# Kernel tuning notes

Hardware: AMD Instinct MI355X
Metric: run time of the kernel (lower is better)

The kernel has to match this reference:

```python
import jax, jax.numpy as jnp
import numpy as np

N = 50000        # nodes
R = 51           # enriched relations (25 fwd + 25 inverse + self-loop)
F_IN = 32        # feat_size
E = 32           # embed_size
C = 16           # num_classes
B = 30           # num_bases
NNZ = 2_000_000  # nonzeros in vertical adjacency


def _xavier(key, shape):
    # mimics nn.init.xavier_uniform_ with gain for relu (sqrt(2))
    fan_in, fan_out = shape[-2], shape[-1]
    a = np.sqrt(2.0) * np.sqrt(6.0 / (fan_in + fan_out))
    return jax.random.uniform(key, shape, jnp.float32, -a, a)


def setup_inputs() -> dict:
    key = jax.random.key(0)
    ks = jax.random.split(key, 8)
    # COO of vertical adjacency, shape (R*N, N)
    rows = jax.random.randint(ks[0], (NNZ,), 0, R * N)
    cols = jax.random.randint(ks[1], (NNZ,), 0, N)
    # row-normalized values: vals = 1 / row_degree  (sum_sparse with rows=True)
    deg = jax.ops.segment_sum(jnp.ones((NNZ,), jnp.float32), rows, num_segments=R * N)
    vals = (1.0 / jnp.maximum(deg, 1.0))[rows]
    features = jax.random.normal(ks[2], (N, F_IN), jnp.float32)
    comps1 = _xavier(ks[3], (R, B))
    bases1 = _xavier(ks[4], (B, F_IN, E))
    comps2 = _xavier(ks[5], (R, B))
    bases2 = _xavier(ks[6], (B, E, C))
    bias1 = jnp.zeros((E,), jnp.float32)
    bias2 = jnp.zeros((C,), jnp.float32)
    return {
        "features": features, "vals": vals,
        "comps1": comps1, "bases1": bases1, "bias1": bias1,
        "comps2": comps2, "bases2": bases2, "bias2": bias2,
        "rows": rows, "cols": cols,
    }


def _spmm(rows, cols, vals, x):
    # (R*N, N) sparse @ (N, f) dense -> (R*N, f)
    return jax.ops.segment_sum(vals[:, None] * x[cols], rows, num_segments=R * N)


def reference(features, vals, comps1, bases1, bias1, comps2, bases2, bias2, rows, cols):
    # layer 1: SpMM then basis-decomposed per-relation mixing
    h = _spmm(rows, cols, vals, features).reshape(R, N, F_IN)   # (r, n, f)
    w1 = jnp.einsum('rb,bfe->rfe', comps1, bases1)              # (r, f, e)
    h = jnp.einsum('rnf,rfe->ne', h, w1)                        # (n, e)
    h = jax.nn.relu(h + bias1)
    # layer 2
    h = _spmm(rows, cols, vals, h).reshape(R, N, E)             # (r, n, e)
    w2 = jnp.einsum('rb,bho->rho', comps2, bases2)              # (r, e, c)
    h = jnp.einsum('rho,rnh->no', w2, h)                        # (n, c)
    return h + bias2
```

## Files before the change

### kernel.cpp

```cpp
#include <hip/hip_runtime.h>

#define NNODES 50000
#define RREL 51
#define FIN 32
#define EDIM 32
#define CDIM 16
#define BB 30
#define NNZ_ 2000000
#define EPB 4096
#define NBUK 391
#define PCAP_MAX 2800128

typedef unsigned int uint32;
typedef unsigned short ushort;
typedef uint32 u32x2 __attribute__((ext_vector_type(2)));
typedef uint32 u32x4 __attribute__((ext_vector_type(4)));
typedef short bf16x8 __attribute__((ext_vector_type(8)));
typedef float f32x4 __attribute__((ext_vector_type(4)));
typedef float f32x16 __attribute__((ext_vector_type(16)));

static __device__ __forceinline__ uint32 pack_bf16x2(float a, float b) {
    uint32 ua = __builtin_bit_cast(uint32, a);
    uint32 ub = __builtin_bit_cast(uint32, b);
    ua += 0x7fffu + ((ua >> 16) & 1u);
    ub += 0x7fffu + ((ub >> 16) & 1u);
    return (ua >> 16) | (ub & 0xffff0000u);
}
static __device__ __forceinline__ ushort bf16_1(float x) {
    uint32 u = __builtin_bit_cast(uint32, x);
    u += 0x7fffu + ((u >> 16) & 1u);
    return (ushort)(u >> 16);
}

__global__ void k_weights2(const float* __restrict__ bases1, const float* __restrict__ bases2,
                           ushort* __restrict__ Wb1, ushort* __restrict__ Wb2) {
    int i = blockIdx.x * 256 + threadIdx.x;
    if (i < 960 * 32) {
        int e = i & 31, k = i >> 5;
        int b = k >> 5, f = k & 31;
        float v = bases1[b * 1024 + f * 32 + e];
        Wb1[((k >> 3) * 32 + e) * 8 + (k & 7)] = bf16_1(v);
    }
    if (i < 960 * 16) {
        int e = i & 15, k = i >> 4;
        int b = k >> 5, h = k & 31;
        float v = bases2[b * 512 + h * 16 + e];
        Wb2[((k >> 3) * 16 + e) * 8 + (k & 7)] = bf16_1(v);
    }
}

__global__ void k_tobf16(const float2* __restrict__ src, uint32* __restrict__ dst, int n2) {
    int i = blockIdx.x * 256 + threadIdx.x;
    if (i < n2) {
        float2 f = src[i];
        dst[i] = pack_bf16x2(f.x, f.y);
    }
}

__global__ __launch_bounds__(1024) void k_bukhist(const int* __restrict__ rows,
                                                  int* __restrict__ buk_cnt) {
    __shared__ int lc[NBUK];
    int t = threadIdx.x;
    if (t < NBUK) lc[t] = 0;
    __syncthreads();
    size_t k = (size_t)blockIdx.x * EPB + (size_t)t * 4;
    int rr[4];
    if (k + 4 <= NNZ_) {
        int4 rw = *(const int4*)(rows + k);
        rr[0] = rw.x; rr[1] = rw.y; rr[2] = rw.z; rr[3] = rw.w;
    } else {
#pragma unroll
        for (int j = 0; j < 4; j++) rr[j] = (k + j < NNZ_) ? rows[k + j] : -1;
    }
#pragma unroll
    for (int j = 0; j < 4; j++)
        if (rr[j] >= 0) {
            int rel = rr[j] / NNODES;
            int dst = rr[j] - rel * NNODES;
            atomicAdd(&lc[dst >> 7], 1);
        }
    __syncthreads();
    if (t < NBUK) atomicAdd(&buk_cnt[t], lc[t]);
}

__global__ void k_scan1(const int* __restrict__ buk_cnt, int* __restrict__ buk_base,
                        int* __restrict__ buk_cur) {
    if (threadIdx.x == 0) {
        int a = 0;
        for (int b = 0; b < NBUK; b++) { buk_base[b] = a; buk_cur[b] = a; a += buk_cnt[b]; }
        buk_base[NBUK] = a;
    }
}

__global__ __launch_bounds__(1024) void k_bucket2(const int* __restrict__ rows,
                                                  const int* __restrict__ cols,
                                                  const float* __restrict__ vals,
                                                  int* __restrict__ buk_cur,
                                                  u32x2* __restrict__ tok8,
                                                  float* __restrict__ sval_b) {
    __shared__ int bukc[NBUK], lb[NBUK], gb[NBUK];
    __shared__ int ssum[1024];
    __shared__ u32x2 st8[EPB];
    __shared__ float sv[EPB];
    int t = threadIdx.x;
    size_t base = (size_t)blockIdx.x * EPB;
    int total = (int)(((size_t)NNZ_ - base < (size_t)EPB) ? ((size_t)NNZ_ - base) : (size_t)EPB);
    if (t < NBUK) bukc[t] = 0;
    __syncthreads();
    size_t k = base + (size_t)t * 4;
    int bv[4]; uint32 tx[4], ty[4]; float vv[4];
    if (k + 4 <= NNZ_) {
        int4 rw = *(const int4*)(rows + k);
        int4 cw = *(const int4*)(cols + k);
        float4 vw = *(const float4*)(vals + k);
        int rr[4] = {rw.x, rw.y, rw.z, rw.w};
        int cc[4] = {cw.x, cw.y, cw.z, cw.w};
        vv[0] = vw.x; vv[1] = vw.y; vv[2] = vw.z; vv[3] = vw.w;
#pragma unroll
        for (int j = 0; j < 4; j++) {
            int rel = rr[j] / NNODES;
            int dst = rr[j] - rel * NNODES;
            bv[j] = dst >> 7;
            tx[j] = (uint32)dst | ((uint32)rel << 16);
            ty[j] = (uint32)cc[j] | ((uint32)rel << 16);
        }
    } else {
#pragma unroll
        for (int j = 0; j < 4; j++) {
            if (k + j < NNZ_) {
                int r = rows[k + j];
                int rel = r / NNODES;
                int dst = r - rel * NNODES;
                bv[j] = dst >> 7;
                tx[j] = (uint32)dst | ((uint32)rel << 16);
                ty[j] = (uint32)cols[k + j] | ((uint32)rel << 16);
                vv[j] = vals[k + j];
            } else bv[j] = -1;
        }
    }
#pragma unroll
    for (int j = 0; j < 4; j++)
        if (bv[j] >= 0) atomicAdd(&bukc[bv[j]], 1);
    __syncthreads();
    int v = (t < NBUK) ? bukc[t] : 0;
    ssum[t] = v;
    __syncthreads();
    for (int off = 1; off < 1024; off <<= 1) {
        int u = (t >= off) ? ssum[t - off] : 0;
        __syncthreads();
        ssum[t] += u;
        __syncthreads();
    }
    if (t < NBUK) { lb[t] = ssum[t] - v; gb[t] = atomicAdd(&buk_cur[t], v); }
    __syncthreads();
    if (t < NBUK) bukc[t] = 0;
    __syncthreads();
#pragma unroll
    for (int j = 0; j < 4; j++) {
        if (bv[j] >= 0) {
            int slot = lb[bv[j]] + atomicAdd(&bukc[bv[j]], 1);
            u32x2 w; w.x = tx[j]; w.y = ty[j];
            st8[slot] = w;
            sv[slot] = vv[j];
        }
    }
    __syncthreads();
    for (int s = t; s < total; s += 1024) {
        u32x2 w = st8[s];
        int bk = (int)((w.x & 0xFFFFu) >> 7);
        int pos = gb[bk] + (s - lb[bk]);
        tok8[pos] = w;
        sval_b[pos] = sv[s];
    }
}

__global__ __launch_bounds__(256) void k_rank3a(const u32x2* __restrict__ tok8,
                                                const int* __restrict__ buk_base,
                                                int* __restrict__ pbuk_cnt) {
    __shared__ int lcnt[128];
    __shared__ int tot;
    int b = blockIdx.x, t = threadIdx.x;
    if (t < 128) lcnt[t] = 0;
    if (t == 0) tot = 0;
    __syncthreads();
    int lo = buk_base[b], hi = buk_base[b + 1];
    for (int i = lo + t; i < hi; i += 256) atomicAdd(&lcnt[tok8[i].x & 127], 1);
    __syncthreads();
    if (t < 128) {
        int d = (b << 7) + t;
        int v = (lcnt[t] + 15) & ~15;
        if (d < NNODES && v == 0) v = 16;
        if (d >= NNODES) v = 0;
        atomicAdd(&tot, v);
    }
    __syncthreads();
    if (t == 0) pbuk_cnt[b] = tot;
}

__global__ void k_scan2(const int* __restrict__ pbuk_cnt, int* __restrict__ pbuk_base) {
    if (threadIdx.x == 0) {
        int a = 0;
        for (int b = 0; b < NBUK; b++) { pbuk_base[b] = a; a += pbuk_cnt[b]; }
        pbuk_base[NBUK] = a;
    }
}

__global__ __launch_bounds__(256) void k_place(const u32x2* __restrict__ tok8,
                                               const float* __restrict__ sval_b,
                                               const int* __restrict__ buk_base,
                                               const int* __restrict__ pbuk_base,
                                               int* __restrict__ pdst_base,
                                               uint32* __restrict__ pe_sr,
                                               float* __restrict__ pe_val) {
    __shared__ int lcnt[128], lexc[128], lrank[128], ssc[128];
    int b = blockIdx.x, t = threadIdx.x;
    int lo = buk_base[b], hi = buk_base[b + 1], pb = pbuk_base[b];
    if (t < 128) { lcnt[t] = 0; lrank[t] = 0; }
    __syncthreads();
    for (int i = lo + t; i < hi; i += 256) atomicAdd(&lcnt[tok8[i].x & 127], 1);
    __syncthreads();
    int v = 0;
    if (t < 128) {
        int d = (b << 7) + t;
        v = (lcnt[t] + 15) & ~15;
        if (d < NNODES && v == 0) v = 16;
        if (d >= NNODES) v = 0;
        ssc[t] = v;
    }
    __syncthreads();
    for (int off = 1; off < 128; off <<= 1) {
        int u = (t >= off && t < 128) ? ssc[t - off] : 0;
        __syncthreads();
        if (t < 128) ssc[t] += u;
        __syncthreads();
    }
    if (t < 128) {
        lexc[t] = ssc[t] - v;
        int d = (b << 7) + t;
        if (d <= NNODES + 4) pdst_base[d] = pb + lexc[t];
    }
    __syncthreads();
    for (int i = lo + t; i < hi; i += 256) {
        u32x2 w = tok8[i];
        int dl = (int)(w.x & 127u);
        int pos = pb + lexc[dl] + atomicAdd(&lrank[dl], 1);
        pe_sr[pos] = w.y;
        pe_val[pos] = sval_b[i];
    }
    if (t < 128) {
        int s0 = pb + lexc[t] + lcnt[t];
        int s1 = pb + lexc[t] + v;
        for (int i = s0; i < s1; i++) { pe_sr[i] = 0u; pe_val[i] = 0.f; }
    }
}

template <int FO, bool RELU, bool BF16OUT>
__global__ __launch_bounds__(256) void k_fused(const uint32* __restrict__ pe_sr,
                                               const float* __restrict__ pe_val,
                                               const int* __restrict__ pdst_base,
                                               const u32x4* __restrict__ Xb,
                                               const u32x4* __restrict__ Wb,
                                               const float* __restrict__ comps,
                                               const float* __restrict__ bias,
                                               void* __restrict__ outp) {
    __shared__ ushort comps_lb[RREL * 32];
    __shared__ uint32 eds[4][64];
    __shared__ __align__(16) ushort xst[4][4][512];
    __shared__ __align__(16) ushort ubuf[4][4][968];
    int t = threadIdx.x, lane = t & 63, wv = t >> 6;
    for (int i = t; i < RREL * 32; i += 256) {
        int r = i >> 5, b = i & 31;
        comps_lb[i] = (b < BB) ? bf16_1(comps[r * BB + b]) : (ushort)0;
    }
    __syncthreads();
    int m = lane & 31, hf = lane >> 5, k0 = hf * 8;
    int ln15 = lane & 15, quad = lane >> 4;
    int d0 = (blockIdx.x * 4 + wv) * 8;
    if (d0 >= NNODES) return;

    auto ccprep = [&](int wi) -> u32x4 {
        uint32 c[8];
#pragma unroll
        for (int j = 0; j < 8; j++) {
            uint32 sr = eds[wv][wi * 16 + k0 + j];
            c[j] = (uint32)comps_lb[((sr >> 16) << 5) | m];
        }
        u32x4 r = { c[0] | (c[1] << 16), c[2] | (c[3] << 16),
                    c[4] | (c[5] << 16), c[6] | (c[7] << 16) };
        return r;
    };
    auto scale8 = [&](u32x4 g, float vm) -> u32x4 {
        u32x4 r;
#pragma unroll
        for (int q = 0; q < 4; q++) {
            float lo = __builtin_bit_cast(float, g[q] << 16) * vm;
            float hi = __builtin_bit_cast(float, g[q] & 0xffff0000u) * vm;
            r[q] = pack_bf16x2(lo, hi);
        }
        return r;
    };
    auto dowin = [&](int wi, u32x4 avq, f32x16 a) -> f32x16 {
        const ushort* xs = &xst[wv][wi][0];
        uint32 b0 = (uint32)xs[(k0 + 0) * 32 + m] | ((uint32)xs[(k0 + 1) * 32 + m] << 16);
        uint32 b1 = (uint32)xs[(k0 + 2) * 32 + m] | ((uint32)xs[(k0 + 3) * 32 + m] << 16);
        uint32 b2 = (uint32)xs[(k0 + 4) * 32 + m] | ((uint32)xs[(k0 + 5) * 32 + m] << 16);
        uint32 b3 = (uint32)xs[(k0 + 6) * 32 + m] | ((uint32)xs[(k0 + 7) * 32 + m] << 16);
        u32x4 bvq = { b0, b1, b2, b3 };
        return __builtin_amdgcn_mfma_f32_32x32x16_bf16(
            __builtin_bit_cast(bf16x8, avq), __builtin_bit_cast(bf16x8, bvq), a, 0, 0, 0);
    };
    auto gather4 = [&](uint32 ps, u32x4& g0, u32x4& g1, u32x4& g2, u32x4& g3) {
        int s0_ = __shfl((int)ps, (lane >> 2), 64);
        g0 = Xb[(size_t)((uint32)s0_ & 0xFFFFu) * 4 + (lane & 3)];
        int s1_ = __shfl((int)ps, 16 + (lane >> 2), 64);
        g1 = Xb[(size_t)((uint32)s1_ & 0xFFFFu) * 4 + (lane & 3)];
        int s2_ = __shfl((int)ps, 32 + (lane >> 2), 64);
        g2 = Xb[(size_t)((uint32)s2_ & 0xFFFFu) * 4 + (lane & 3)];
        int s3_ = __shfl((int)ps, 48 + (lane >> 2), 64);
        g3 = Xb[(size_t)((uint32)s3_ & 0xFFFFu) * 4 + (lane & 3)];
    };

    int A0 = pdst_base[d0];
    int e1_ = pdst_base[d0 + 1];
    int A1 = A0 + 64; if (A1 > e1_) A1 = e1_;
    uint32 pvsC = __builtin_nontemporal_load(&pe_sr[A0 + lane]);
    float  pvvC = __builtin_nontemporal_load(&pe_val[A0 + lane]);
    uint32 pvsN = __builtin_nontemporal_load(&pe_sr[A1 + lane]);
    float  pvvN = __builtin_nontemporal_load(&pe_val[A1 + lane]);
    u32x4 gx0, gx1, gx2, gx3, gy0, gy1, gy2, gy3;
    gather4(pvsC, gx0, gx1, gx2, gx3);

#pragma unroll 1
    for (int batch = 0; batch < 2; batch++) {
        int db = d0 + batch * 4;
#pragma unroll 1
        for (int s = 0; s < 4; s++) {
            int d = db + s;
            int lo = pdst_base[d], segEnd = pdst_base[d + 1], e2 = pdst_base[d + 2];
            f32x16 acc;
#pragma unroll
            for (int i = 0; i < 16; i++) acc[i] = 0.f;
#pragma unroll 1
            for (int c0 = lo; c0 < segEnd; c0 += 64) {
                int aN = c0 + 64; if (aN > segEnd) aN = segEnd;
                int lim = (aN == segEnd) ? e2 : segEnd;
                int aNN = aN + 64; if (aNN > lim) aNN = lim;
                uint32 pvsP = __builtin_nontemporal_load(&pe_sr[aNN + lane]);
                float  pvvP = __builtin_nontemporal_load(&pe_val[aNN + lane]);
                gather4(pvsN, gy0, gy1, gy2, gy3);
                eds[wv][lane] = pvsC;
                int nwin = (segEnd - c0) >> 4;
                if (nwin > 4) nwin = 4;
                u32x4 av0, av1, av2, av3;
                av0 = ccprep(0);
                if (nwin > 1) av1 = ccprep(1);
                if (nwin > 2) av2 = ccprep(2);
                if (nwin > 3) av3 = ccprep(3);
                {
                    float vm = __shfl(pvvC, (lane >> 2), 64);
                    *(u32x4*)&xst[wv][0][lane * 8] = scale8(gx0, vm);
                }
                if (nwin > 1) {
                    float vm = __shfl(pvvC, 16 + (lane >> 2), 64);
                    *(u32x4*)&xst[wv][1][lane * 8] = scale8(gx1, vm);
                }
                if (nwin > 2) {
                    float vm = __shfl(pvvC, 32 + (lane >> 2), 64);
                    *(u32x4*)&xst[wv][2][lane * 8] = scale8(gx2, vm);
                }
                if (nwin > 3) {
                    float vm = __shfl(pvvC, 48 + (lane >> 2), 64);
                    *(u32x4*)&xst[wv][3][lane * 8] = scale8(gx3, vm);
                }
                acc = dowin(0, av0, acc);
                if (nwin > 1) acc = dowin(1, av1, acc);
                if (nwin > 2) acc = dowin(2, av2, acc);
                if (nwin > 3) acc = dowin(3, av3, acc);
                gx0 = gy0; gx1 = gy1; gx2 = gy2; gx3 = gy3;
                pvsC = pvsN; pvvC = pvvN; pvsN = pvsP; pvvN = pvvP;
            }
#pragma unroll
            for (int r = 0; r < 16; r++) {
                int b = (r & 3) + 8 * (r >> 2) + 4 * hf;
                float vme = acc[r];
                float vot = __shfl_xor(vme, 1, 64);
                if (b < BB && !(m & 1)) {
                    *(uint32*)&ubuf[wv][s][b * 32 + m] = pack_bf16x2(vme, vot);
                }
            }
        }
        const int NT = FO / 16;
        f32x4 a2[NT];
#pragma unroll
        for (int tt = 0; tt < NT; tt++)
#pragma unroll
            for (int i = 0; i < 4; i++) a2[tt][i] = 0.f;
#pragma unroll 6
        for (int ks = 0; ks < 30; ks++) {
            bf16x8 af = *(const bf16x8*)&ubuf[wv][ln15 & 3][ks * 32 + quad * 8];
#pragma unroll
            for (int tt = 0; tt < NT; tt++) {
                bf16x8 bf2 = __builtin_bit_cast(bf16x8, Wb[(ks * 4 + quad) * FO + ln15 + 16 * tt]);
                a2[tt] = __builtin_amdgcn_mfma_f32_16x16x32_bf16(af, bf2, a2[tt], 0, 0, 0);
            }
        }
        if (quad == 0) {
#pragma unroll
            for (int r = 0; r < 4; r++) {
                int dst = db + r;
                if (dst < NNODES) {
                    if (BF16OUT) {
                        ushort* hp = (ushort*)outp;
#pragma unroll
                        for (int tt = 0; tt < NT; tt++) {
                            float o = a2[tt][r] + bias[ln15 + 16 * tt];
                            if (RELU) o = fmaxf(o, 0.f);
                            hp[(size_t)dst * FO + ln15 + 16 * tt] = bf16_1(o);
                        }
                    } else {
                        float o = a2[0][r] + bias[ln15];
                        if (RELU) o = fmaxf(o, 0.f);
                        ((float*)outp)[(size_t)dst * FO + ln15] = o;
                    }
                }
            }
        }
    }
}

extern "C" void kernel_launch(void* const* d_in, const int* in_sizes, int n_in,
                              void* d_out, int out_size, void* d_ws, size_t ws_size,
                              hipStream_t stream) {
    const float* features = (const float*)d_in[0];
    const float* vals     = (const float*)d_in[1];
    const float* comps1   = (const float*)d_in[2];
    const float* bases1   = (const float*)d_in[3];
    const float* bias1    = (const float*)d_in[4];
    const float* comps2   = (const float*)d_in[5];
    const float* bases2   = (const float*)d_in[6];
    const float* bias2    = (const float*)d_in[7];
    const int*   rows     = (const int*)d_in[8];
    const int*   cols     = (const int*)d_in[9];
    float* out = (float*)d_out;

    float* ws = (float*)d_ws;
    size_t o = 0;
    ushort* Wb1 = (ushort*)(ws + o); o += 960 * 32 / 2;
    ushort* Wb2 = (ushort*)(ws + o); o += 960 * 16 / 2;
    uint32* Xb  = (uint32*)(ws + o); o += (size_t)NNODES * 16;
    uint32* h1b = (uint32*)(ws + o); o += (size_t)NNODES * 16;
    uint32* pe_sr  = (uint32*)(ws + o); o += PCAP_MAX;
    float*  pe_val = (float*)(ws + o);  o += PCAP_MAX;
    int* pdst_base = (int*)(ws + o); o += NNODES + 8;
    int* buk_cnt   = (int*)(ws + o); o += NBUK;
    int* buk_base  = (int*)(ws + o); o += NBUK + 1;
    int* buk_cur   = (int*)(ws + o); o += NBUK;
    int* pbuk_cnt  = (int*)(ws + o); o += NBUK;
    int* pbuk_base = (int*)(ws + o); o += NBUK + 1;
    o = (o + 1) & ~(size_t)1;
    u32x2* tok8 = (u32x2*)(ws + o); o += 2 * (size_t)NNZ_;
    float* sval_b = (float*)(ws + o); o += (size_t)NNZ_;

    const int NB = (NNZ_ + EPB - 1) / EPB;

    hipMemsetAsync(buk_cnt, 0, NBUK * sizeof(int), stream);

    k_weights2<<<(960 * 32 + 255) / 256, 256, 0, stream>>>(bases1, bases2, Wb1, Wb2);
    k_tobf16<<<(NNODES * FIN / 2 + 255) / 256, 256, 0, stream>>>((const float2*)features, Xb,
                                                                 NNODES * FIN / 2);
    k_bukhist<<<NB, 1024, 0, stream>>>(rows, buk_cnt);
    k_scan1<<<1, 64, 0, stream>>>(buk_cnt, buk_base, buk_cur);
    k_bucket2<<<NB, 1024, 0, stream>>>(rows, cols, vals, buk_cur, tok8, sval_b);
    k_rank3a<<<NBUK, 256, 0, stream>>>(tok8, buk_base, pbuk_cnt);
    k_scan2<<<1, 64, 0, stream>>>(pbuk_cnt, pbuk_base);
    k_place<<<NBUK, 256, 0, stream>>>(tok8, sval_b, buk_base, pbuk_base, pdst_base, pe_sr, pe_val);

    k_fused<EDIM, true, true><<<(NNODES + 31) / 32, 256, 0, stream>>>(
        pe_sr, pe_val, pdst_base, (const u32x4*)Xb, (const u32x4*)Wb1, comps1, bias1, h1b);
    k_fused<CDIM, false, false><<<(NNODES + 31) / 32, 256, 0, stream>>>(
        pe_sr, pe_val, pdst_base, (const u32x4*)h1b, (const u32x4*)Wb2, comps2, bias2, out);
}
```

Measured before the change: 365.6 us.

## Parallelize bucket scans with wave shuffles and halve per-batch destination count

Replaces the single-thread serial prefix scans over 391 buckets with a 64-lane shuffle-based scan with carry. In the fused SpMM kernel, each wave now processes 4 batches of 2 destinations instead of 2 batches of 4. This halves the ubuf shared-memory staging buffer, which could raise occupancy. The cost is running the second-stage MFMA loop twice as often, with only half its rows carrying useful data.

```diff
diff --git a/kernel.cpp b/kernel.cpp
--- a/kernel.cpp
+++ b/kernel.cpp
@@ -85,11 +85,22 @@
 
 __global__ void k_scan1(const int* __restrict__ buk_cnt, int* __restrict__ buk_base,
                         int* __restrict__ buk_cur) {
-    if (threadIdx.x == 0) {
-        int a = 0;
-        for (int b = 0; b < NBUK; b++) { buk_base[b] = a; buk_cur[b] = a; a += buk_cnt[b]; }
-        buk_base[NBUK] = a;
-    }
+    int t = threadIdx.x;
+    int carry = 0;
+    for (int c = 0; c < NBUK; c += 64) {
+        int idx = c + t;
+        int v = (idx < NBUK) ? buk_cnt[idx] : 0;
+        int sum = v;
+#pragma unroll
+        for (int off = 1; off < 64; off <<= 1) {
+            int u = __shfl_up(sum, off, 64);
+            if (t >= off) sum += u;
+        }
+        int exc = carry + sum - v;
+        if (idx < NBUK) { buk_base[idx] = exc; buk_cur[idx] = exc; }
+        carry += __shfl(sum, 63, 64);
+    }
+    if (t == 0) buk_base[NBUK] = carry;
 }
 
 __global__ __launch_bounds__(1024) void k_bucket2(const int* __restrict__ rows,
@@ -198,11 +209,21 @@
 }
 
 __global__ void k_scan2(const int* __restrict__ pbuk_cnt, int* __restrict__ pbuk_base) {
-    if (threadIdx.x == 0) {
-        int a = 0;
-        for (int b = 0; b < NBUK; b++) { pbuk_base[b] = a; a += pbuk_cnt[b]; }
-        pbuk_base[NBUK] = a;
-    }
+    int t = threadIdx.x;
+    int carry = 0;
+    for (int c = 0; c < NBUK; c += 64) {
+        int idx = c + t;
+        int v = (idx < NBUK) ? pbuk_cnt[idx] : 0;
+        int sum = v;
+#pragma unroll
+        for (int off = 1; off < 64; off <<= 1) {
+            int u = __shfl_up(sum, off, 64);
+            if (t >= off) sum += u;
+        }
+        if (idx < NBUK) pbuk_base[idx] = carry + sum - v;
+        carry += __shfl(sum, 63, 64);
+    }
+    if (t == 0) pbuk_base[NBUK] = carry;
 }
 
 __global__ __launch_bounds__(256) void k_place(const u32x2* __restrict__ tok8,
@@ -266,7 +287,7 @@
     __shared__ ushort comps_lb[RREL * 32];
     __shared__ uint32 eds[4][64];
     __shared__ __align__(16) ushort xst[4][4][512];
-    __shared__ __align__(16) ushort ubuf[4][4][968];
+    __shared__ __align__(16) ushort ubuf[4][2][968];
     int t = threadIdx.x, lane = t & 63, wv = t >> 6;
     for (int i = t; i < RREL * 32; i += 256) {
         int r = i >> 5, b = i & 31;
@@ -331,10 +352,10 @@
     gather4(pvsC, gx0, gx1, gx2, gx3);
 
 #pragma unroll 1
-    for (int batch = 0; batch < 2; batch++) {
-        int db = d0 + batch * 4;
+    for (int batch = 0; batch < 4; batch++) {
+        int db = d0 + batch * 2;
 #pragma unroll 1
-        for (int s = 0; s < 4; s++) {
+        for (int s = 0; s < 2; s++) {
             int d = db + s;
             int lo = pdst_base[d], segEnd = pdst_base[d + 1], e2 = pdst_base[d + 2];
             f32x16 acc;
@@ -397,7 +418,7 @@
             for (int i = 0; i < 4; i++) a2[tt][i] = 0.f;
 #pragma unroll 6
         for (int ks = 0; ks < 30; ks++) {
-            bf16x8 af = *(const bf16x8*)&ubuf[wv][ln15 & 3][ks * 32 + quad * 8];
+            bf16x8 af = *(const bf16x8*)&ubuf[wv][ln15 & 1][ks * 32 + quad * 8];
 #pragma unroll
             for (int tt = 0; tt < NT; tt++) {
                 bf16x8 bf2 = __builtin_bit_cast(bf16x8, Wb[(ks * 4 + quad) * FO + ln15 + 16 * tt]);
@@ -406,7 +427,7 @@
         }
         if (quad == 0) {
 #pragma unroll
-            for (int r = 0; r < 4; r++) {
+            for (int r = 0; r < 2; r++) {
                 int dst = db + r;
                 if (dst < NNODES) {
                     if (BF16OUT) {
```

After: 403.4 us. 10.4% more time.
